# Kernel tuning notes

Measured on AMD Instinct MI355X. Metric: run time of the kernel, lower is better.

The kernel has to match this reference:

```python
import jax, jax.numpy as jnp
import numpy as np

GAMMA = 0.9865


def setup_inputs() -> dict:
    key = jax.random.key(0)
    ks = jax.random.split(key, 6)
    B, T, DIN, D = 8, 2048, 1024, 1024
    return {
        "xq": jax.random.normal(ks[0], (B, T, DIN), dtype=jnp.float32),
        "xk": jax.random.normal(ks[1], (B, T, DIN), dtype=jnp.float32),
        "xv": jax.random.normal(ks[2], (B, T, DIN), dtype=jnp.float32),
        "Wq": jax.random.normal(ks[3], (DIN, D), dtype=jnp.float32) * (DIN ** -0.5),
        "Wk": jax.random.normal(ks[4], (DIN, D), dtype=jnp.float32) * (DIN ** -0.5),
        "Wv": jax.random.normal(ks[5], (DIN, D), dtype=jnp.float32) * (DIN ** -0.5),
    }


def reference(xq, xk, xv, Wq, Wk, Wv):
    # Dense projections (no bias)
    Q = jnp.einsum("btd,de->bte", xq, Wq)  # [B,T,D]
    K = jnp.einsum("btd,de->bte", xk, Wk)
    V = jnp.einsum("btd,de->bte", xv, Wv)

    # einsum('ib,bj->bj', K_t^T, V_t) == (sum_i K[b,t,i]) * V[b,t,:]
    ksum = jnp.sum(K, axis=-1)            # [B,T]
    u = ksum[..., None] * V               # [B,T,D]
    # recurrence starts at t=1 with s[0]=0, so u[0] never contributes
    u = u * (jnp.arange(u.shape[1]) > 0)[None, :, None]

    def step(s, u_t):
        s = s * jnp.float32(GAMMA) + u_t
        return s, s

    s0 = jnp.zeros(u.shape[::2], dtype=u.dtype)          # [B,D]
    _, S = jax.lax.scan(step, s0, jnp.swapaxes(u, 0, 1))  # S: [T,B,D]
    return Q * jnp.swapaxes(S, 0, 1)                      # [B,T,D]
```

## Files before the change

### kernel.cpp

```cpp
#include <hip/hip_runtime.h>
#include <hip/hip_bf16.h>

#define GAMMA 0.9865f

typedef __attribute__((ext_vector_type(8))) short bf16x8;
typedef __attribute__((ext_vector_type(4))) float f32x4;

static constexpr int Bb  = 8;
static constexpr int Tt  = 2048;
static constexpr int DIN = 1024;
static constexpr int Dd  = 1024;
static constexpr int Mm  = Bb * Tt;
static constexpr int CL  = 64;
static constexpr int NC  = Tt / CL;
static constexpr int NT  = DIN / 64;

__device__ __forceinline__ void gload16(const void* g, void* l) {
  __builtin_amdgcn_global_load_lds(
      (const __attribute__((address_space(1))) void*)g,
      (__attribute__((address_space(3))) void*)l, 16, 0, 0);
}

__device__ __forceinline__ void bar() {
  asm volatile("" ::: "memory");
  __builtin_amdgcn_s_barrier();
  asm volatile("" ::: "memory");
}

__global__ void wsum_kernel(const float* __restrict__ Wk, float* __restrict__ wsum) {
  int row  = blockIdx.x * 4 + (threadIdx.x >> 6);
  int lane = threadIdx.x & 63;
  const float4* rp = (const float4*)(Wk + (size_t)row * DIN);
  float s = 0.f;
#pragma unroll
  for (int i = 0; i < 4; ++i) {
    float4 v = rp[lane + i * 64];
    s += v.x + v.y + v.z + v.w;
  }
  for (int off = 32; off; off >>= 1) s += __shfl_down(s, off);
  if (lane == 0) wsum[row] = s;
}

__global__ void wt_kernel(const float* __restrict__ Wq, const float* __restrict__ Wv,
                          __hip_bfloat16* __restrict__ Wt) {
  const float* W = blockIdx.z ? Wv : Wq;
  __hip_bfloat16* outp = Wt + (size_t)blockIdx.z * DIN * Dd;
  __shared__ float tile[32][33];
  int k0 = blockIdx.x * 32, n0 = blockIdx.y * 32;
  int tx = threadIdx.x, ty = threadIdx.y;
#pragma unroll
  for (int i = 0; i < 4; ++i)
    tile[ty + i * 8][tx] = W[(size_t)(k0 + ty + i * 8) * Dd + n0 + tx];
  __syncthreads();
#pragma unroll
  for (int i = 0; i < 4; ++i)
    outp[(size_t)(n0 + ty + i * 8) * DIN + k0 + tx] =
        __float2bfloat16(tile[tx][ty + i * 8]);
}

__global__ __launch_bounds__(256) void cast_kernel(
    const float* __restrict__ xq, const float* __restrict__ xv,
    __hip_bfloat16* __restrict__ oq, __hip_bfloat16* __restrict__ ov) {
  const float* src = blockIdx.y ? xv : xq;
  __hip_bfloat16* dst = blockIdx.y ? ov : oq;
  size_t i = (size_t)blockIdx.x * 256 + threadIdx.x;
  const float4* p = (const float4*)src;
  float4 a = p[i * 2], b = p[i * 2 + 1];
  union { __hip_bfloat16 h[8]; bf16x8 v; } u;
  u.h[0] = __float2bfloat16(a.x); u.h[1] = __float2bfloat16(a.y);
  u.h[2] = __float2bfloat16(a.z); u.h[3] = __float2bfloat16(a.w);
  u.h[4] = __float2bfloat16(b.x); u.h[5] = __float2bfloat16(b.y);
  u.h[6] = __float2bfloat16(b.z); u.h[7] = __float2bfloat16(b.w);
  ((bf16x8*)dst)[i] = u.v;
}


__device__ __forceinline__ void stage_half(const __hip_bfloat16* g, char* l, int tid) {
#pragma unroll
  for (int j = 0; j < 2; ++j) {
    int c = tid + j * 512;
    int row = c >> 3, ch = c & 7;
    gload16(g + (size_t)row * DIN + ((ch ^ (row & 7)) << 3), l + c * 16);
  }
}

__device__ __forceinline__ bf16x8 lds_frag(const char* base, int row, int kc) {
  return *(const bf16x8*)(base + (((row << 3) + (kc ^ (row & 7))) << 4));
}

#define MFMA_QUAD(MLO, NLO)                                                  \
  _Pragma("unroll") for (int mi = 0; mi < 4; ++mi)                           \
  _Pragma("unroll") for (int ni = 0; ni < 2; ++ni)                           \
  _Pragma("unroll") for (int ks = 0; ks < 2; ++ks)                           \
      acc[(MLO) + mi][(NLO) + ni] = __builtin_amdgcn_mfma_f32_16x16x32_bf16( \
          a[(MLO) + mi][ks], b[(NLO) + ni][ks], acc[(MLO) + mi][(NLO) + ni], 0, 0, 0);

__global__ __launch_bounds__(512, 2) void gemm8_kernel(
    const __hip_bfloat16* __restrict__ Aq, const __hip_bfloat16* __restrict__ Av,
    const __hip_bfloat16* __restrict__ Wt,
    __hip_bfloat16* __restrict__ Qbf, __hip_bfloat16* __restrict__ Vbf) {
  extern __shared__ char lds[];

  int lin = blockIdx.x;
  int wg  = (lin & 7) * 64 + (lin >> 3);
  int z   = wg >> 8, rem = wg & 255;
  int by  = rem & 3, bx = rem >> 2;

  const __hip_bfloat16* Ab = z ? Av : Aq;
  const int m0 = bx * 256, n0 = by * 256;
  const __hip_bfloat16* Ag = Ab + (size_t)m0 * DIN;
  const __hip_bfloat16* Bg = Wt + ((size_t)z * Dd + n0) * DIN;
  __hip_bfloat16* Cc = z ? Vbf : Qbf;

  const int tid = threadIdx.x;
  const int wv = tid >> 6, lane = tid & 63;
  const int wm = (wv >> 2) * 128, wn = (wv & 3) * 64;
  const int fq = lane >> 4, fr = lane & 15;

  f32x4 acc[8][4] = {};

  stage_half(Ag,                  lds,                 tid);
  stage_half(Ag + 128 * DIN,      lds + 16384,         tid);
  stage_half(Bg,                  lds + 32768,         tid);
  stage_half(Bg + 128 * DIN,      lds + 49152,         tid);
  stage_half(Ag + 64,             lds + 65536,         tid);
  stage_half(Ag + 128 * DIN + 64, lds + 65536 + 16384, tid);
  asm volatile("s_waitcnt vmcnt(4)" ::: "memory");
  bar();

  for (int t = 0; t < NT; ++t) {
    char* buf  = lds + (t & 1) * 65536;
    char* bufN = lds + ((t + 1) & 1) * 65536;
    const char* At = buf;
    const char* Bt = buf + 32768;
    bf16x8 a[8][2], b[4][2];

#pragma unroll
    for (int mi = 0; mi < 4; ++mi)
#pragma unroll
      for (int ks = 0; ks < 2; ++ks)
        a[mi][ks] = lds_frag(At, wm + mi * 16 + fr, ks * 4 + fq);
#pragma unroll
    for (int ni = 0; ni < 2; ++ni)
#pragma unroll
      for (int ks = 0; ks < 2; ++ks)
        b[ni][ks] = lds_frag(Bt, wn + ni * 16 + fr, ks * 4 + fq);
    if (t + 1 < NT) stage_half(Bg + (size_t)(t + 1) * 64, bufN + 32768, tid);
    bar();
    __builtin_amdgcn_s_setprio(1);
    MFMA_QUAD(0, 0);
    __builtin_amdgcn_s_setprio(0);
    bar();

#pragma unroll
    for (int mi = 4; mi < 8; ++mi)
#pragma unroll
      for (int ks = 0; ks < 2; ++ks)
        a[mi][ks] = lds_frag(At, wm + mi * 16 + fr, ks * 4 + fq);
    if (t + 1 < NT)
      stage_half(Bg + 128 * DIN + (size_t)(t + 1) * 64, bufN + 49152, tid);
    bar();
    __builtin_amdgcn_s_setprio(1);
    MFMA_QUAD(4, 0);
    __builtin_amdgcn_s_setprio(0);
    bar();

#pragma unroll
    for (int ni = 2; ni < 4; ++ni)
#pragma unroll
      for (int ks = 0; ks < 2; ++ks)
        b[ni][ks] = lds_frag(Bt, wn + ni * 16 + fr, ks * 4 + fq);
    if (t + 2 < NT) stage_half(Ag + (size_t)(t + 2) * 64, buf, tid);
    bar();
    __builtin_amdgcn_s_setprio(1);
    MFMA_QUAD(0, 2);
    __builtin_amdgcn_s_setprio(0);
    bar();

    if (t + 2 < NT)
      stage_half(Ag + 128 * DIN + (size_t)(t + 2) * 64, buf + 16384, tid);
    if (t + 1 < NT) {
      if (t + 2 < NT) asm volatile("s_waitcnt vmcnt(4)" ::: "memory");
      else            asm volatile("s_waitcnt vmcnt(0)" ::: "memory");
    }
    bar();
    __builtin_amdgcn_s_setprio(1);
    MFMA_QUAD(4, 2);
    __builtin_amdgcn_s_setprio(0);
    bar();
  }

#pragma unroll
  for (int mi = 0; mi < 8; ++mi) {
#pragma unroll
    for (int ni = 0; ni < 4; ++ni) {
      f32x4 v = acc[mi][ni];
      int row = m0 + wm + mi * 16 + fq * 4;
      int col = n0 + wn + ni * 16 + fr;
#pragma unroll
      for (int j = 0; j < 4; ++j)
        Cc[(size_t)(row + j) * Dd + col] = __float2bfloat16(v[j]);
    }
  }
}

__global__ void ksum_kernel(const float* __restrict__ xk, const float* __restrict__ wsum,
                            float* __restrict__ ksum) {
  int row  = blockIdx.x * 4 + (threadIdx.x >> 6);
  int lane = threadIdx.x & 63;
  const float4* rp = (const float4*)(xk + (size_t)row * DIN);
  const float4* wp = (const float4*)wsum;
  float s = 0.f;
#pragma unroll
  for (int i = 0; i < 4; ++i) {
    float4 a = rp[lane + i * 64];
    float4 w = wp[lane + i * 64];
    s += a.x * w.x + a.y * w.y + a.z * w.z + a.w * w.w;
  }
  for (int off = 32; off; off >>= 1) s += __shfl_down(s, off);
  if (lane == 0) ksum[row] = s;
}

__global__ void scanA_kernel(const __hip_bfloat16* __restrict__ Vbf,
                             const float* __restrict__ ksum,
                             float* __restrict__ E) {
  int b = blockIdx.x, c = blockIdx.y;
  int d = blockIdx.z * 256 + threadIdx.x;
  const __hip_bfloat16* Vp = Vbf + ((size_t)(b * Tt + c * CL) * Dd) + d;
  const float* kp = ksum + b * Tt + c * CL;
  float s = 0.f;
#pragma unroll 8
  for (int t = 0; t < CL; ++t) {
    float u = kp[t] * __bfloat162float(Vp[(size_t)t * Dd]);
    if (c == 0 && t == 0) u = 0.f;
    s = s * GAMMA + u;
  }
  E[((size_t)b * NC + c) * Dd + d] = s;
}

__global__ void scanB_kernel(const float* __restrict__ E, float* __restrict__ carry,
                             float gCL) {
  int b = blockIdx.x;
  int d = blockIdx.y * 256 + threadIdx.x;
  float send = 0.f;
  for (int c = 0; c < NC; ++c) {
    size_t idx = ((size_t)b * NC + c) * Dd + d;
    float e = E[idx];
    carry[idx] = send;
    send = e + gCL * send;
  }
}

__global__ void final_kernel(const __hip_bfloat16* __restrict__ Vbf,
                             const __hip_bfloat16* __restrict__ Qbf,
                             const float* __restrict__ ksum,
                             const float* __restrict__ carry,
                             float* __restrict__ outp) {
  int b = blockIdx.x, c = blockIdx.y;
  int d = blockIdx.z * 256 + threadIdx.x;
  size_t base = ((size_t)(b * Tt + c * CL) * Dd) + d;
  float s = carry[((size_t)b * NC + c) * Dd + d];
  const float* kp = ksum + b * Tt + c * CL;
#pragma unroll 4
  for (int t = 0; t < CL; ++t) {
    float u = kp[t] * __bfloat162float(Vbf[base + (size_t)t * Dd]);
    if (c == 0 && t == 0) u = 0.f;
    s = s * GAMMA + u;
    outp[base + (size_t)t * Dd] = __bfloat162float(Qbf[base + (size_t)t * Dd]) * s;
  }
}

extern "C" void kernel_launch(void* const* d_in, const int* in_sizes, int n_in,
                              void* d_out, int out_size, void* d_ws, size_t ws_size,
                              hipStream_t stream) {
  (void)in_sizes; (void)n_in; (void)out_size; (void)ws_size;
  const float* xq = (const float*)d_in[0];
  const float* xk = (const float*)d_in[1];
  const float* xv = (const float*)d_in[2];
  const float* Wq = (const float*)d_in[3];
  const float* Wk = (const float*)d_in[4];
  const float* Wv = (const float*)d_in[5];
  float* outp = (float*)d_out;

  char* ws = (char*)d_ws;
  size_t off = 0;
  auto alloc = [&](size_t bytes) {
    char* p = ws + off;
    off += (bytes + 255) & ~(size_t)255;
    return p;
  };
  __hip_bfloat16* xq_bf = (__hip_bfloat16*)alloc((size_t)Mm * DIN * 2);
  __hip_bfloat16* xv_bf = (__hip_bfloat16*)alloc((size_t)Mm * DIN * 2);
  __hip_bfloat16* Wt    = (__hip_bfloat16*)alloc((size_t)2 * DIN * Dd * 2);
  __hip_bfloat16* Qbf   = (__hip_bfloat16*)alloc((size_t)Mm * Dd * 2);
  __hip_bfloat16* Vbf   = (__hip_bfloat16*)alloc((size_t)Mm * Dd * 2);
  float* wsum  = (float*)alloc((size_t)DIN * 4);
  float* ksum  = (float*)alloc((size_t)Mm * 4);
  float* E     = (float*)alloc((size_t)Bb * NC * Dd * 4);
  float* carry = (float*)alloc((size_t)Bb * NC * Dd * 4);

  double g = 1.0;
  for (int i = 0; i < CL; ++i) g *= (double)GAMMA;
  float gCL = (float)g;

  (void)hipFuncSetAttribute((const void*)gemm8_kernel,
                            hipFuncAttributeMaxDynamicSharedMemorySize, 131072);

  wsum_kernel<<<DIN / 4, 256, 0, stream>>>(Wk, wsum);
  wt_kernel<<<dim3(DIN / 32, Dd / 32, 2), dim3(32, 8), 0, stream>>>(Wq, Wv, Wt);
  cast_kernel<<<dim3(Mm * DIN / 8 / 256, 2), 256, 0, stream>>>(xq, xv, xq_bf, xv_bf);
  ksum_kernel<<<Mm / 4, 256, 0, stream>>>(xk, wsum, ksum);
  gemm8_kernel<<<512, 512, 131072, stream>>>(xq_bf, xv_bf, Wt, Qbf, Vbf);
  scanA_kernel<<<dim3(Bb, NC, Dd / 256), 256, 0, stream>>>(Vbf, ksum, E);
  scanB_kernel<<<dim3(Bb, Dd / 256), 256, 0, stream>>>(E, carry, gCL);
  final_kernel<<<dim3(Bb, NC, Dd / 256), 256, 0, stream>>>(Vbf, Qbf, ksum, carry, outp);
}
```

Baseline: 157.0 us.

## Vectorize scan/final kernels, nontemporal loads, and two N-tiles per GEMM block

```diff
diff --git a/kernel.cpp b/kernel.cpp
--- a/kernel.cpp
+++ b/kernel.cpp
@@ -5,6 +5,7 @@
 
 typedef __attribute__((ext_vector_type(8))) short bf16x8;
 typedef __attribute__((ext_vector_type(4))) float f32x4;
+typedef __attribute__((ext_vector_type(2))) unsigned int u32x2;
 
 static constexpr int Bb  = 8;
 static constexpr int Tt  = 2048;
@@ -27,6 +28,13 @@
   asm volatile("" ::: "memory");
 }
 
+__device__ __forceinline__ float bflo(unsigned int u) {
+  return __uint_as_float((u & 0xffffu) << 16);
+}
+__device__ __forceinline__ float bfhi(unsigned int u) {
+  return __uint_as_float(u & 0xffff0000u);
+}
+
 __global__ void wsum_kernel(const float* __restrict__ Wk, float* __restrict__ wsum) {
   int row  = blockIdx.x * 4 + (threadIdx.x >> 6);
   int lane = threadIdx.x & 63;
@@ -64,14 +72,18 @@
   const float* src = blockIdx.y ? xv : xq;
   __hip_bfloat16* dst = blockIdx.y ? ov : oq;
   size_t i = (size_t)blockIdx.x * 256 + threadIdx.x;
-  const float4* p = (const float4*)src;
-  float4 a = p[i * 2], b = p[i * 2 + 1];
-  union { __hip_bfloat16 h[8]; bf16x8 v; } u;
-  u.h[0] = __float2bfloat16(a.x); u.h[1] = __float2bfloat16(a.y);
-  u.h[2] = __float2bfloat16(a.z); u.h[3] = __float2bfloat16(a.w);
-  u.h[4] = __float2bfloat16(b.x); u.h[5] = __float2bfloat16(b.y);
-  u.h[6] = __float2bfloat16(b.z); u.h[7] = __float2bfloat16(b.w);
-  ((bf16x8*)dst)[i] = u.v;
+  const f32x4* p = (const f32x4*)src + i * 4;
+  f32x4 f[4];
+#pragma unroll
+  for (int j = 0; j < 4; ++j) f[j] = __builtin_nontemporal_load(p + j);
+  bf16x8* q = (bf16x8*)dst + i * 2;
+#pragma unroll
+  for (int h = 0; h < 2; ++h) {
+    union { __hip_bfloat16 b[8]; bf16x8 v; } u;
+#pragma unroll
+    for (int j = 0; j < 8; ++j) u.b[j] = __float2bfloat16(f[h * 2 + j / 4][j & 3]);
+    __builtin_nontemporal_store(u.v, q + h);
+  }
 }
 
 
@@ -102,14 +114,13 @@
   extern __shared__ char lds[];
 
   int lin = blockIdx.x;
-  int wg  = (lin & 7) * 64 + (lin >> 3);
-  int z   = wg >> 8, rem = wg & 255;
-  int by  = rem & 3, bx = rem >> 2;
+  int wg  = (lin & 7) * 32 + (lin >> 3);
+  int z   = wg >> 7, rem = wg & 127;
+  int byp = rem & 1, bx = rem >> 1;
 
   const __hip_bfloat16* Ab = z ? Av : Aq;
-  const int m0 = bx * 256, n0 = by * 256;
+  const int m0 = bx * 256;
   const __hip_bfloat16* Ag = Ab + (size_t)m0 * DIN;
-  const __hip_bfloat16* Bg = Wt + ((size_t)z * Dd + n0) * DIN;
   __hip_bfloat16* Cc = z ? Vbf : Qbf;
 
   const int tid = threadIdx.x;
@@ -117,89 +128,108 @@
   const int wm = (wv >> 2) * 128, wn = (wv & 3) * 64;
   const int fq = lane >> 4, fr = lane & 15;
 
-  f32x4 acc[8][4] = {};
-
-  stage_half(Ag,                  lds,                 tid);
-  stage_half(Ag + 128 * DIN,      lds + 16384,         tid);
-  stage_half(Bg,                  lds + 32768,         tid);
-  stage_half(Bg + 128 * DIN,      lds + 49152,         tid);
-  stage_half(Ag + 64,             lds + 65536,         tid);
-  stage_half(Ag + 128 * DIN + 64, lds + 65536 + 16384, tid);
-  asm volatile("s_waitcnt vmcnt(4)" ::: "memory");
-  bar();
-
-  for (int t = 0; t < NT; ++t) {
-    char* buf  = lds + (t & 1) * 65536;
-    char* bufN = lds + ((t + 1) & 1) * 65536;
-    const char* At = buf;
-    const char* Bt = buf + 32768;
-    bf16x8 a[8][2], b[4][2];
-
-#pragma unroll
-    for (int mi = 0; mi < 4; ++mi)
-#pragma unroll
-      for (int ks = 0; ks < 2; ++ks)
-        a[mi][ks] = lds_frag(At, wm + mi * 16 + fr, ks * 4 + fq);
-#pragma unroll
-    for (int ni = 0; ni < 2; ++ni)
-#pragma unroll
-      for (int ks = 0; ks < 2; ++ks)
-        b[ni][ks] = lds_frag(Bt, wn + ni * 16 + fr, ks * 4 + fq);
-    if (t + 1 < NT) stage_half(Bg + (size_t)(t + 1) * 64, bufN + 32768, tid);
+  {
+    const __hip_bfloat16* Bg0 = Wt + ((size_t)z * Dd + (size_t)byp * 512) * DIN;
+    stage_half(Ag,                  lds,                 tid);
+    stage_half(Ag + 128 * DIN,      lds + 16384,         tid);
+    stage_half(Bg0,                 lds + 32768,         tid);
+    stage_half(Bg0 + 128 * DIN,     lds + 49152,         tid);
+    stage_half(Ag + 64,             lds + 65536,         tid);
+    stage_half(Ag + 128 * DIN + 64, lds + 65536 + 16384, tid);
+    asm volatile("s_waitcnt vmcnt(4)" ::: "memory");
     bar();
-    __builtin_amdgcn_s_setprio(1);
-    MFMA_QUAD(0, 0);
-    __builtin_amdgcn_s_setprio(0);
-    bar();
-
-#pragma unroll
-    for (int mi = 4; mi < 8; ++mi)
-#pragma unroll
-      for (int ks = 0; ks < 2; ++ks)
-        a[mi][ks] = lds_frag(At, wm + mi * 16 + fr, ks * 4 + fq);
-    if (t + 1 < NT)
-      stage_half(Bg + 128 * DIN + (size_t)(t + 1) * 64, bufN + 49152, tid);
-    bar();
-    __builtin_amdgcn_s_setprio(1);
-    MFMA_QUAD(4, 0);
-    __builtin_amdgcn_s_setprio(0);
-    bar();
-
-#pragma unroll
-    for (int ni = 2; ni < 4; ++ni)
-#pragma unroll
-      for (int ks = 0; ks < 2; ++ks)
-        b[ni][ks] = lds_frag(Bt, wn + ni * 16 + fr, ks * 4 + fq);
-    if (t + 2 < NT) stage_half(Ag + (size_t)(t + 2) * 64, buf, tid);
-    bar();
-    __builtin_amdgcn_s_setprio(1);
-    MFMA_QUAD(0, 2);
-    __builtin_amdgcn_s_setprio(0);
-    bar();
-
-    if (t + 2 < NT)
-      stage_half(Ag + 128 * DIN + (size_t)(t + 2) * 64, buf + 16384, tid);
-    if (t + 1 < NT) {
-      if (t + 2 < NT) asm volatile("s_waitcnt vmcnt(4)" ::: "memory");
-      else            asm volatile("s_waitcnt vmcnt(0)" ::: "memory");
+  }
+
+  for (int rep = 0; rep < 2; ++rep) {
+    const int n0 = (byp * 2 + rep) * 256;
+    const __hip_bfloat16* Bg = Wt + ((size_t)z * Dd + n0) * DIN;
+    f32x4 acc[8][4] = {};
+
+    for (int t = 0; t < NT; ++t) {
+      char* buf  = lds + (t & 1) * 65536;
+      char* bufN = lds + ((t + 1) & 1) * 65536;
+      const char* At = buf;
+      const char* Bt = buf + 32768;
+      bf16x8 a[8][2], b[4][2];
+
+#pragma unroll
+      for (int mi = 0; mi < 4; ++mi)
+#pragma unroll
+        for (int ks = 0; ks < 2; ++ks)
+          a[mi][ks] = lds_frag(At, wm + mi * 16 + fr, ks * 4 + fq);
+#pragma unroll
+      for (int ni = 0; ni < 2; ++ni)
+#pragma unroll
+        for (int ks = 0; ks < 2; ++ks)
+          b[ni][ks] = lds_frag(Bt, wn + ni * 16 + fr, ks * 4 + fq);
+      if (t + 1 < NT) stage_half(Bg + (size_t)(t + 1) * 64, bufN + 32768, tid);
+      bar();
+      __builtin_amdgcn_s_setprio(1);
+      MFMA_QUAD(0, 0);
+      __builtin_amdgcn_s_setprio(0);
+      bar();
+
+#pragma unroll
+      for (int mi = 4; mi < 8; ++mi)
+#pragma unroll
+        for (int ks = 0; ks < 2; ++ks)
+          a[mi][ks] = lds_frag(At, wm + mi * 16 + fr, ks * 4 + fq);
+      if (t + 1 < NT)
+        stage_half(Bg + 128 * DIN + (size_t)(t + 1) * 64, bufN + 49152, tid);
+      bar();
+      __builtin_amdgcn_s_setprio(1);
+      MFMA_QUAD(4, 0);
+      __builtin_amdgcn_s_setprio(0);
+      bar();
+
+#pragma unroll
+      for (int ni = 2; ni < 4; ++ni)
+#pragma unroll
+        for (int ks = 0; ks < 2; ++ks)
+          b[ni][ks] = lds_frag(Bt, wn + ni * 16 + fr, ks * 4 + fq);
+      if (t + 2 < NT) stage_half(Ag + (size_t)(t + 2) * 64, buf, tid);
+      bar();
+      __builtin_amdgcn_s_setprio(1);
+      MFMA_QUAD(0, 2);
+      __builtin_amdgcn_s_setprio(0);
+      bar();
+
+      if (t + 2 < NT)
+        stage_half(Ag + 128 * DIN + (size_t)(t + 2) * 64, buf + 16384, tid);
+      if (t + 1 < NT) {
+        if (t + 2 < NT) asm volatile("s_waitcnt vmcnt(4)" ::: "memory");
+        else            asm volatile("s_waitcnt vmcnt(0)" ::: "memory");
+      }
+      bar();
+      __builtin_amdgcn_s_setprio(1);
+      MFMA_QUAD(4, 2);
+      __builtin_amdgcn_s_setprio(0);
+      bar();
     }
-    bar();
-    __builtin_amdgcn_s_setprio(1);
-    MFMA_QUAD(4, 2);
-    __builtin_amdgcn_s_setprio(0);
-    bar();
-  }
-
-#pragma unroll
-  for (int mi = 0; mi < 8; ++mi) {
-#pragma unroll
-    for (int ni = 0; ni < 4; ++ni) {
-      f32x4 v = acc[mi][ni];
-      int row = m0 + wm + mi * 16 + fq * 4;
-      int col = n0 + wn + ni * 16 + fr;
-#pragma unroll
-      for (int j = 0; j < 4; ++j)
-        Cc[(size_t)(row + j) * Dd + col] = __float2bfloat16(v[j]);
+
+#pragma unroll
+    for (int mi = 0; mi < 8; ++mi) {
+#pragma unroll
+      for (int ni = 0; ni < 4; ++ni) {
+        f32x4 v = acc[mi][ni];
+        int row = m0 + wm + mi * 16 + fq * 4;
+        int col = n0 + wn + ni * 16 + fr;
+#pragma unroll
+        for (int j = 0; j < 4; ++j)
+          Cc[(size_t)(row + j) * Dd + col] = __float2bfloat16(v[j]);
+      }
+    }
+
+    if (rep == 0) {
+      const __hip_bfloat16* Bg1 = Wt + ((size_t)z * Dd + (size_t)(byp * 2 + 1) * 256) * DIN;
+      stage_half(Ag,                  lds,                 tid);
+      stage_half(Ag + 128 * DIN,      lds + 16384,         tid);
+      stage_half(Bg1,                 lds + 32768,         tid);
+      stage_half(Bg1 + 128 * DIN,     lds + 49152,         tid);
+      stage_half(Ag + 64,             lds + 65536,         tid);
+      stage_half(Ag + 128 * DIN + 64, lds + 65536 + 16384, tid);
+      asm volatile("s_waitcnt vmcnt(4)" ::: "memory");
+      bar();
     }
   }
 }
@@ -208,34 +238,39 @@
                             float* __restrict__ ksum) {
   int row  = blockIdx.x * 4 + (threadIdx.x >> 6);
   int lane = threadIdx.x & 63;
-  const float4* rp = (const float4*)(xk + (size_t)row * DIN);
+  const f32x4* rp = (const f32x4*)(xk + (size_t)row * DIN);
   const float4* wp = (const float4*)wsum;
   float s = 0.f;
 #pragma unroll
   for (int i = 0; i < 4; ++i) {
-    float4 a = rp[lane + i * 64];
+    f32x4 a = __builtin_nontemporal_load(rp + lane + i * 64);
     float4 w = wp[lane + i * 64];
-    s += a.x * w.x + a.y * w.y + a.z * w.z + a.w * w.w;
+    s += a[0] * w.x + a[1] * w.y + a[2] * w.z + a[3] * w.w;
   }
   for (int off = 32; off; off >>= 1) s += __shfl_down(s, off);
   if (lane == 0) ksum[row] = s;
 }
 
-__global__ void scanA_kernel(const __hip_bfloat16* __restrict__ Vbf,
-                             const float* __restrict__ ksum,
-                             float* __restrict__ E) {
+__global__ __launch_bounds__(256) void scanA_kernel(
+    const __hip_bfloat16* __restrict__ Vbf, const float* __restrict__ ksum,
+    float* __restrict__ E) {
   int b = blockIdx.x, c = blockIdx.y;
-  int d = blockIdx.z * 256 + threadIdx.x;
-  const __hip_bfloat16* Vp = Vbf + ((size_t)(b * Tt + c * CL) * Dd) + d;
+  int d0 = threadIdx.x * 4;
+  const __hip_bfloat16* Vp = Vbf + ((size_t)(b * Tt + c * CL) * Dd) + d0;
   const float* kp = ksum + b * Tt + c * CL;
-  float s = 0.f;
-#pragma unroll 8
+  float s0 = 0.f, s1 = 0.f, s2 = 0.f, s3 = 0.f;
+#pragma unroll 4
   for (int t = 0; t < CL; ++t) {
-    float u = kp[t] * __bfloat162float(Vp[(size_t)t * Dd]);
-    if (c == 0 && t == 0) u = 0.f;
-    s = s * GAMMA + u;
-  }
-  E[((size_t)b * NC + c) * Dd + d] = s;
+    u32x2 r = __builtin_nontemporal_load((const u32x2*)(Vp + (size_t)t * Dd));
+    float kv = kp[t];
+    if (c == 0 && t == 0) kv = 0.f;
+    s0 = s0 * GAMMA + kv * bflo(r.x);
+    s1 = s1 * GAMMA + kv * bfhi(r.x);
+    s2 = s2 * GAMMA + kv * bflo(r.y);
+    s3 = s3 * GAMMA + kv * bfhi(r.y);
+  }
+  f32x4 e; e[0] = s0; e[1] = s1; e[2] = s2; e[3] = s3;
+  *(f32x4*)(E + ((size_t)b * NC + c) * Dd + d0) = e;
 }
 
 __global__ void scanB_kernel(const float* __restrict__ E, float* __restrict__ carry,
@@ -251,22 +286,33 @@
   }
 }
 
-__global__ void final_kernel(const __hip_bfloat16* __restrict__ Vbf,
-                             const __hip_bfloat16* __restrict__ Qbf,
-                             const float* __restrict__ ksum,
-                             const float* __restrict__ carry,
-                             float* __restrict__ outp) {
+__global__ __launch_bounds__(256) void final_kernel(
+    const __hip_bfloat16* __restrict__ Vbf, const __hip_bfloat16* __restrict__ Qbf,
+    const float* __restrict__ ksum, const float* __restrict__ carry,
+    float* __restrict__ outp) {
   int b = blockIdx.x, c = blockIdx.y;
-  int d = blockIdx.z * 256 + threadIdx.x;
-  size_t base = ((size_t)(b * Tt + c * CL) * Dd) + d;
-  float s = carry[((size_t)b * NC + c) * Dd + d];
+  int d0 = threadIdx.x * 4;
+  size_t base = ((size_t)(b * Tt + c * CL) * Dd) + d0;
+  f32x4 cr = *(const f32x4*)(carry + ((size_t)b * NC + c) * Dd + d0);
+  float s0 = cr[0], s1 = cr[1], s2 = cr[2], s3 = cr[3];
   const float* kp = ksum + b * Tt + c * CL;
 #pragma unroll 4
   for (int t = 0; t < CL; ++t) {
-    float u = kp[t] * __bfloat162float(Vbf[base + (size_t)t * Dd]);
-    if (c == 0 && t == 0) u = 0.f;
-    s = s * GAMMA + u;
-    outp[base + (size_t)t * Dd] = __bfloat162float(Qbf[base + (size_t)t * Dd]) * s;
+    size_t o = base + (size_t)t * Dd;
+    u32x2 rv = __builtin_nontemporal_load((const u32x2*)(Vbf + o));
+    u32x2 rq = __builtin_nontemporal_load((const u32x2*)(Qbf + o));
+    float kv = kp[t];
+    if (c == 0 && t == 0) kv = 0.f;
+    s0 = s0 * GAMMA + kv * bflo(rv.x);
+    s1 = s1 * GAMMA + kv * bfhi(rv.x);
+    s2 = s2 * GAMMA + kv * bflo(rv.y);
+    s3 = s3 * GAMMA + kv * bfhi(rv.y);
+    f32x4 ov;
+    ov[0] = bflo(rq.x) * s0;
+    ov[1] = bfhi(rq.x) * s1;
+    ov[2] = bflo(rq.y) * s2;
+    ov[3] = bfhi(rq.y) * s3;
+    __builtin_nontemporal_store(ov, (f32x4*)(outp + o));
   }
 }
 
@@ -308,10 +354,10 @@
 
   wsum_kernel<<<DIN / 4, 256, 0, stream>>>(Wk, wsum);
   wt_kernel<<<dim3(DIN / 32, Dd / 32, 2), dim3(32, 8), 0, stream>>>(Wq, Wv, Wt);
-  cast_kernel<<<dim3(Mm * DIN / 8 / 256, 2), 256, 0, stream>>>(xq, xv, xq_bf, xv_bf);
+  cast_kernel<<<dim3(Mm * DIN / 16 / 256, 2), 256, 0, stream>>>(xq, xv, xq_bf, xv_bf);
   ksum_kernel<<<Mm / 4, 256, 0, stream>>>(xk, wsum, ksum);
-  gemm8_kernel<<<512, 512, 131072, stream>>>(xq_bf, xv_bf, Wt, Qbf, Vbf);
-  scanA_kernel<<<dim3(Bb, NC, Dd / 256), 256, 0, stream>>>(Vbf, ksum, E);
+  gemm8_kernel<<<256, 512, 131072, stream>>>(xq_bf, xv_bf, Wt, Qbf, Vbf);
+  scanA_kernel<<<dim3(Bb, NC), 256, 0, stream>>>(Vbf, ksum, E);
   scanB_kernel<<<dim3(Bb, Dd / 256), 256, 0, stream>>>(E, carry, gCL);
-  final_kernel<<<dim3(Bb, NC, Dd / 256), 256, 0, stream>>>(Vbf, Qbf, ksum, carry, outp);
-}
+  final_kernel<<<dim3(Bb, NC), 256, 0, stream>>>(Vbf, Qbf, ksum, carry, outp);
+}
```

After: 191.1 us. +21.7%, slower.
